# Kernel tuning notes

Measured on AMD Instinct MI355X. Metric: run time of the kernel, lower is better.

Reference implementation:

```python
import jax, jax.numpy as jnp
import numpy as np

ANGLE_SCALE = 100.0
DIST_SCALE = 100.0
DIST_BOUNDARY = 0.0
HID = 128
N_HIDDEN = 2  # output_layer
EPS = 1e-08


def _mlp(x, w0, b0, ws, bs):
    # Linear, then N_HIDDEN x (ReLU, Linear)
    h = x @ w0 + b0
    for i in range(ws.shape[0]):
        h = jax.nn.relu(h) @ ws[i] + bs[i]
    return h


def _capsule_endpoints(x):
    # x: [..., 9] -> A, B endpoints of capsule segment, radius r
    c, s = jnp.cos(x[..., 3:4] * ANGLE_SCALE), jnp.sin(x[..., 3:4] * ANGLE_SCALE)
    half = x[..., 2:3] / 2
    ctr = x[..., 0:2]
    off = jnp.concatenate([half * c, half * s], axis=-1)
    return ctr - off, ctr + off, x[..., 4:5]


def _pt_seg_dist(P, A, AB, AB_sq):
    t = jnp.clip(((P - A) * AB).sum(-1, keepdims=True) / AB_sq, 0.0, 1.0)
    Q = A + t * AB
    return jnp.linalg.norm(P - Q, axis=-1, keepdims=True)


def _dist_to_capsule(init_e, query_e):
    A1, B1, r1 = _capsule_endpoints(init_e)
    A2, B2, r2 = _capsule_endpoints(query_e)
    A1B1, A2B2 = B1 - A1, B2 - A2
    s1 = (A1B1 ** 2).sum(-1, keepdims=True) + EPS
    s2 = (A2B2 ** 2).sum(-1, keepdims=True) + EPS
    d = jnp.minimum(
        jnp.minimum(_pt_seg_dist(A2, A1, A1B1, s1), _pt_seg_dist(B2, A1, A1B1, s1)),
        jnp.minimum(_pt_seg_dist(A1, A2, A2B2, s2), _pt_seg_dist(B1, A2, A2B2, s2)),
    )
    return d - r1 - r2


def setup_inputs() -> dict:
    key = jax.random.key(0)
    ks = jax.random.split(key, 32)
    B, O, T = 64, 64, 64
    f = lambda k, shp, scale=1.0: jax.random.normal(k, shp, dtype=jnp.float32) * scale
    inp = {
        'init_x': f(ks[0], (B, O, 9)),
        'query_x': f(ks[1], (B, T, 9)),
        'init_v': f(ks[2], (B, O, 2)),
        'query_v': f(ks[3], (B, T, 2)),
        'init_angular_v': f(ks[4], (B, O, 1)),
        'query_angular_v': f(ks[5], (B, T, 1)),
        'trunk_w0': f(ks[6], (9, HID), 0.3), 'trunk_b0': f(ks[7], (HID,), 0.1),
        'trunk_ws': f(ks[8], (N_HIDDEN, HID, HID), 0.08), 'trunk_bs': f(ks[9], (N_HIDDEN, HID), 0.1),
        'branch_w0': f(ks[10], (5, HID), 0.3), 'branch_b0': f(ks[11], (HID,), 0.1),
        'branch_ws': f(ks[12], (N_HIDDEN, HID, HID), 0.08), 'branch_bs': f(ks[13], (N_HIDDEN, HID), 0.1),
        'out_w': f(ks[14], (HID, 3), 0.08), 'out_b': f(ks[15], (3,), 0.1),
        'spring_w0': f(ks[16], (1, HID), 0.3), 'spring_b0': f(ks[17], (HID,), 0.1),
        'spring_w1': f(ks[18], (HID, 1), 0.08), 'spring_b1': f(ks[19], (1,), 0.1),
        'joint_w0': f(ks[20], (15, HID), 0.3), 'joint_b0': f(ks[21], (HID,), 0.1),
        'joint_w1': f(ks[22], (HID, 2), 0.08), 'joint_b1': f(ks[23], (2,), 0.1),
    }
    return inp


def reference(init_x, query_x, init_v, query_v, init_angular_v, query_angular_v,
              trunk_w0, trunk_b0, trunk_ws, trunk_bs,
              branch_w0, branch_b0, branch_ws, branch_bs,
              out_w, out_b, spring_w0, spring_b0, spring_w1, spring_b1,
              joint_w0, joint_b0, joint_w1, joint_b1):
    B, O, _ = init_x.shape
    T = query_x.shape[1]
    # pairwise broadcast: init along obj axis (dim1), query along target axis (dim2)
    init_e = jnp.broadcast_to(init_x[:, :, None, :], (B, O, T, 9))
    query_e = jnp.broadcast_to(query_x[:, None, :, :], (B, O, T, 9))
    rel = query_e[..., :2] - init_e[..., :2]
    query_e = jnp.concatenate([rel, query_e[..., 2:]], axis=-1)
    init_e = jnp.concatenate([jnp.zeros_like(rel), init_e[..., 2:]], axis=-1)
    qv = query_v[:, None, :, :] - init_v[:, :, None, :]           # [B,O,T,2]
    qav = query_angular_v[:, None, :, :] - init_angular_v[:, :, None, :]  # [B,O,T,1]
    iav = jnp.broadcast_to(init_angular_v[:, :, None, :], (B, O, T, 1))

    dist = _dist_to_capsule(init_e, query_e)
    dist_mask = (dist <= DIST_BOUNDARY).astype(jnp.float32)
    dist_input = dist * dist_mask * DIST_SCALE

    branch_in = init_e[..., :5]
    trunk_in = jnp.concatenate([query_e[..., :5], qv, qav, dist_input], axis=-1)
    branch_out = _mlp(branch_in, branch_w0, branch_b0, branch_ws, branch_bs)
    trunk_out = _mlp(trunk_in, trunk_w0, trunk_b0, trunk_ws, trunk_bs)
    force = (branch_out * trunk_out) @ out_w + out_b  # [B,O,T,3]

    # spring force
    have_spring = ((init_e[..., 8:9] == query_e[..., 8:9]) & (init_e[..., 8:9] > 0)).astype(jnp.float32)
    dvec = init_e[..., :2] - query_e[..., :2]
    length = jnp.linalg.norm(dvec, axis=-1, keepdims=True)
    dvec = dvec / (length + EPS)
    sf = jax.nn.relu(length @ spring_w0 + spring_b0) @ spring_w1 + spring_b1  # [B,O,T,1]
    sf = sf * dvec
    sf = jnp.concatenate([sf, jnp.zeros_like(sf[..., :1])], axis=-1) * have_spring

    # joint force (torch .long() truncates toward zero)
    i7, q7 = init_e[..., 7:8], query_e[..., 7:8]
    have_joint = ((jnp.trunc(i7) == jnp.trunc(q7)) & (i7 > 0)).astype(jnp.float32)
    joint_in = jnp.concatenate([init_e[..., :5], query_e[..., :5], qv, iav, qav, i7 - jnp.trunc(i7)], axis=-1)
    jf = jax.nn.relu(joint_in @ joint_w0 + joint_b0) @ joint_w1 + joint_b1  # [B,O,T,2]
    jf = jf * have_joint
    jf = jnp.concatenate([jf, jnp.zeros_like(jf[..., :1])], axis=-1)

    force = force * dist_mask + sf + jf
    return force
```

## Files before the change

kernel.cpp:

```cpp
#include <hip/hip_runtime.h>
#include <math.h>


typedef _Float16 h4v __attribute__((ext_vector_type(4)));
typedef _Float16 h8v __attribute__((ext_vector_type(8)));
typedef float    f4v __attribute__((ext_vector_type(4)));
typedef unsigned int u32;

#define TW0_OFF 0
#define JW0_OFF 4096
#define TWS_OFF 8192
#define BW0_OFF 40960
#define BWS_OFF 45056
#define W_TOTAL 77824
#define BR_OFF_F (W_TOTAL/2)

#define FRAG_BLOCKS 304
#define BR_BLOCKS   256

__global__ __launch_bounds__(256)
void prep_kernel(const float* __restrict__ tw0, const float* __restrict__ tws,
                 const float* __restrict__ jw0, const float* __restrict__ bw0,
                 const float* __restrict__ bws, const float* __restrict__ bb0,
                 const float* __restrict__ bbs, const float* __restrict__ init_x,
                 _Float16* __restrict__ wsH, float* __restrict__ brw)
{
    __shared__ float bsm[2*16*132];
    const int tid = threadIdx.x;

    if (blockIdx.x < FRAG_BLOCKS) {
        int idx = blockIdx.x * 256 + tid;
        if (idx >= W_TOTAL) return;
        const int j = idx & 7;
        const int lane = (idx >> 3) & 63;
        const int q = lane >> 4, r = lane & 15;
        _Float16 v;
        if (idx < JW0_OFF) {
            int mt = idx >> 9;
            int k = q*8 + j, m = mt*16 + r;
            v = (k < 9) ? (_Float16)tw0[k*128 + m] : (_Float16)0.f;
        } else if (idx < TWS_OFF) {
            int mt = (idx - JW0_OFF) >> 9;
            int k = q*8 + j, m = mt*16 + r;
            v = (k < 15) ? (_Float16)jw0[k*128 + m] : (_Float16)0.f;
        } else if (idx < BW0_OFF) {
            int e = idx - TWS_OFF;
            int ks = (e >> 9) & 3, mt = (e >> 11) & 7, l = e >> 14;
            int k = ks*32 + q*8 + j, m = mt*16 + r;
            v = (_Float16)tws[l*16384 + k*128 + m];
        } else if (idx < BWS_OFF) {
            int mt = (idx - BW0_OFF) >> 9;
            int k = q*8 + j, m = mt*16 + r;
            v = (k < 5) ? (_Float16)bw0[k*128 + m] : (_Float16)0.f;
        } else {
            int e = idx - BWS_OFF;
            int ks = (e >> 9) & 3, mt = (e >> 11) & 7, l = e >> 14;
            int k = ks*32 + q*8 + j, m = mt*16 + r;
            v = (_Float16)bws[l*16384 + k*128 + m];
        }
        wsH[idx] = v;
        return;
    }

    const int blk2 = blockIdx.x - FRAG_BLOCKS;
    const int row0 = blk2*16;
    const int lane = tid & 63, w = tid >> 6;
    const int q = lane >> 4, r = lane & 15;
    float* h0 = bsm;
    float* h1 = bsm + 16*132;

    for (int e = tid; e < 2048; e += 256) {
        const int rw = e >> 7, n = e & 127;
        const float* ixp = init_x + (row0 + rw)*9;
        float acc = bb0[n];
        acc = fmaf(ixp[2], bw0[2*128 + n], acc);
        acc = fmaf(ixp[3], bw0[3*128 + n], acc);
        acc = fmaf(ixp[4], bw0[4*128 + n], acc);
        h0[rw*132 + n] = acc;
    }
    __syncthreads();

    #pragma unroll
    for (int L = 0; L < 2; ++L) {
        const float* Wg = bws + L*16384;
        const float* bi = bbs + L*128;
        const float* in = (L == 0) ? h0 : h1;
        #pragma unroll
        for (int mi = 0; mi < 2; ++mi) {
            const int mt = w + mi*4;
            const int m0 = mt*16 + q*4;
            h8v af[4];
            #pragma unroll
            for (int ks = 0; ks < 4; ++ks)
                #pragma unroll
                for (int j = 0; j < 8; ++j)
                    af[ks][j] = (_Float16)Wg[(ks*32 + q*8 + j)*128 + mt*16 + r];
            f4v acc = *(const f4v*)&bi[m0];
            #pragma unroll
            for (int ks = 0; ks < 4; ++ks) {
                f4v x0 = *(const f4v*)&in[r*132 + ks*32 + q*8];
                f4v x1 = *(const f4v*)&in[r*132 + ks*32 + q*8 + 4];
                h8v bf;
                #pragma unroll
                for (int i = 0; i < 4; ++i) {
                    bf[i]   = (_Float16)fmaxf(x0[i], 0.f);
                    bf[4+i] = (_Float16)fmaxf(x1[i], 0.f);
                }
                acc = __builtin_amdgcn_mfma_f32_16x16x32_f16(af[ks], bf, acc, 0, 0, 0);
            }
            if (L == 0)
                *(f4v*)&h1[r*132 + m0] = acc;
            else
                *(f4v*)&brw[(row0 + r)*128 + m0] = acc;
        }
        __syncthreads();
    }
}

__device__ __forceinline__ u32 sh_u32(u32 v, int idx) {
    return (u32)__shfl((int)v, idx, 64);
}
__device__ __forceinline__ h8v make_h8(u32 a, u32 b, u32 c, u32 d) {
    union { u32 u[4]; h8v h; } t;
    t.u[0] = a; t.u[1] = b; t.u[2] = c; t.u[3] = d;
    return t.h;
}
__device__ __forceinline__ u32 pack_relu2(float x, float y) {
    union { _Float16 h[2]; u32 u; } t;
    t.h[0] = (_Float16)fmaxf(x, 0.f);
    t.h[1] = (_Float16)fmaxf(y, 0.f);
    return t.u;
}

#define BUILD_BF(dst, P) do {                                                 \
    _Pragma("unroll")                                                         \
    for (int ks_ = 0; ks_ < 4; ++ks_) {                                       \
        u32 lo0 = sh_u32((P)[2*ks_][0],   idxA);                              \
        u32 hi0 = sh_u32((P)[2*ks_+1][0], idxA);                              \
        u32 lo1 = sh_u32((P)[2*ks_][1],   idxA);                              \
        u32 hi1 = sh_u32((P)[2*ks_+1][1], idxA);                              \
        u32 lo2 = sh_u32((P)[2*ks_][0],   idxB);                              \
        u32 hi2 = sh_u32((P)[2*ks_+1][0], idxB);                              \
        u32 lo3 = sh_u32((P)[2*ks_][1],   idxB);                              \
        u32 hi3 = sh_u32((P)[2*ks_+1][1], idxB);                              \
        (dst)[ks_] = make_h8(hiSel ? hi0 : lo0, hiSel ? hi1 : lo1,            \
                             hiSel ? hi2 : lo2, hiSel ? hi3 : lo3);           \
    }                                                                         \
} while (0)

__global__ __launch_bounds__(64)
void ff_kernel(const float* __restrict__ init_x,  const float* __restrict__ query_x,
               const float* __restrict__ init_v,  const float* __restrict__ query_v,
               const float* __restrict__ init_av, const float* __restrict__ query_av,
               const float* __restrict__ tb0, const float* __restrict__ tbs,
               const float* __restrict__ out_w, const float* __restrict__ out_b,
               const float* __restrict__ sw0, const float* __restrict__ sb0,
               const float* __restrict__ sw1, const float* __restrict__ sb1,
               const float* __restrict__ jb0,
               const float* __restrict__ jw1, const float* __restrict__ jb1,
               const _Float16* __restrict__ wsH, const float* __restrict__ brw,
               float* __restrict__ out)
{
    const int lane = threadIdx.x;
    const int bid  = blockIdx.x;
    const int obid = bid >> 1;
    const int half = bid & 1;
    const int b    = obid >> 6;
    const int g    = lane >> 4, c = lane & 15;
    const int idxA = (g & 1)*32 + c;
    const int idxB = idxA + 16;
    const bool hiSel = (lane & 32) != 0;

    const float* ix = init_x + obid*9;
    const float ix0 = ix[0], ix1 = ix[1], ix2 = ix[2], ix3 = ix[3], ix4 = ix[4];
    const float ix7 = ix[7], ix8 = ix[8];
    float s1v, c1v; sincosf(ix3 * 100.f, &s1v, &c1v);
    const float hh1 = ix2 * 0.5f;
    const float o1x = hh1*c1v, o1y = hh1*s1v;
    const float A1x = -o1x, A1y = -o1y;
    const float ab1x = 2.f*o1x, ab1y = 2.f*o1y;
    const float s1sq = ab1x*ab1x + ab1y*ab1y + 1e-8f;
    const float iv0 = init_v[obid*2+0], iv1 = init_v[obid*2+1];
    const float iav = init_av[obid];
    const float i7t = truncf(ix7);
    const float fr7 = ix7 - i7t;

    u32  p[2][8][2];
    float mask_[2], dvx_[2], dvy_[2], hs_[2], hj_[2], len_[2];
    float jf0_[2], jf1_[2];

    #pragma unroll
    for (int ntl = 0; ntl < 2; ++ntl) {
        const int tq = (half*2 + ntl)*16 + c;
        const float* qx = query_x + (b*64 + tq)*9;
        const float qx0 = qx[0], qx1 = qx[1], qx2 = qx[2], qx3 = qx[3], qx4 = qx[4];
        const float qx7 = qx[7], qx8 = qx[8];
        const float rel0 = qx0 - ix0, rel1 = qx1 - ix1;

        float s2v, c2v; sincosf(qx3 * 100.f, &s2v, &c2v);
        const float hh2 = qx2 * 0.5f;
        const float o2x = hh2*c2v, o2y = hh2*s2v;
        const float A2x = rel0 - o2x, A2y = rel1 - o2y;
        const float B2x = rel0 + o2x, B2y = rel1 + o2y;
        const float ab2x = 2.f*o2x, ab2y = 2.f*o2y;
        const float s2sq = ab2x*ab2x + ab2y*ab2y + 1e-8f;

        float Px, Py, Ax, Ay, ABx, ABy, ss;
        if (g < 2) {
            Ax = A1x; Ay = A1y; ABx = ab1x; ABy = ab1y; ss = s1sq;
            Px = (g == 0) ? A2x : B2x;  Py = (g == 0) ? A2y : B2y;
        } else {
            Ax = A2x; Ay = A2y; ABx = ab2x; ABy = ab2y; ss = s2sq;
            Px = (g == 2) ? A1x : o1x;  Py = (g == 2) ? A1y : o1y;
        }
        float t = ((Px - Ax)*ABx + (Py - Ay)*ABy) / ss;
        t = fminf(fmaxf(t, 0.f), 1.f);
        const float dx = Px - (Ax + t*ABx);
        const float dy = Py - (Ay + t*ABy);
        float dq = sqrtf(dx*dx + dy*dy);
        dq = fminf(dq, __shfl_xor(dq, 16));
        dq = fminf(dq, __shfl_xor(dq, 32));

        const float dist = dq - ix4 - qx4;
        const float mask = (dist <= 0.f) ? 1.f : 0.f;
        const float dinp = dist * mask * 100.f;
        const float qv0 = query_v[(b*64+tq)*2+0] - iv0;
        const float qv1 = query_v[(b*64+tq)*2+1] - iv1;
        const float qav = query_av[b*64+tq] - iav;
        const float len = sqrtf(rel0*rel0 + rel1*rel1);
        const float inv = 1.f / (len + 1e-8f);

        mask_[ntl] = mask;
        dvx_[ntl]  = -rel0 * inv;
        dvy_[ntl]  = -rel1 * inv;
        hs_[ntl]   = ((ix8 == qx8) && (ix8 > 0.f)) ? 1.f : 0.f;
        hj_[ntl]   = ((i7t == truncf(qx7)) && (ix7 > 0.f)) ? 1.f : 0.f;
        len_[ntl]  = len;

        const bool g0 = (g == 0), g1 = (g == 1);
        h8v bT, bJ;
        bT[0] = (_Float16)(g0 ? rel0 : g1 ? dinp : 0.f);
        bT[1] = (_Float16)(g0 ? rel1 : 0.f);
        bT[2] = (_Float16)(g0 ? qx2  : 0.f);
        bT[3] = (_Float16)(g0 ? qx3  : 0.f);
        bT[4] = (_Float16)(g0 ? qx4  : 0.f);
        bT[5] = (_Float16)(g0 ? qv0  : 0.f);
        bT[6] = (_Float16)(g0 ? qv1  : 0.f);
        bT[7] = (_Float16)(g0 ? qav  : 0.f);
        bJ[0] = (_Float16)(g1 ? qx3  : 0.f);
        bJ[1] = (_Float16)(g1 ? qx4  : 0.f);
        bJ[2] = (_Float16)(g0 ? ix2  : g1 ? qv0 : 0.f);
        bJ[3] = (_Float16)(g0 ? ix3  : g1 ? qv1 : 0.f);
        bJ[4] = (_Float16)(g0 ? ix4  : g1 ? iav : 0.f);
        bJ[5] = (_Float16)(g0 ? rel0 : g1 ? qav : 0.f);
        bJ[6] = (_Float16)(g0 ? rel1 : g1 ? fr7 : 0.f);
        bJ[7] = (_Float16)(g0 ? qx2  : 0.f);

        float jf0 = 0.f, jf1 = 0.f;
        #pragma unroll
        for (int mt = 0; mt < 8; ++mt) {
            const int m0 = mt*16 + g*4;
            h8v aT = *(const h8v*)&wsH[TW0_OFF + (mt*64 + lane)*8];
            f4v accT = *(const f4v*)&tb0[m0];
            accT = __builtin_amdgcn_mfma_f32_16x16x32_f16(aT, bT, accT, 0, 0, 0);
            p[ntl][mt][0] = pack_relu2(accT[0], accT[1]);
            p[ntl][mt][1] = pack_relu2(accT[2], accT[3]);

            h8v aJ = *(const h8v*)&wsH[JW0_OFF + (mt*64 + lane)*8];
            f4v accJ = *(const f4v*)&jb0[m0];
            accJ = __builtin_amdgcn_mfma_f32_16x16x32_f16(aJ, bJ, accJ, 0, 0, 0);
            f4v jwa = *(const f4v*)&jw1[m0*2];
            f4v jwb = *(const f4v*)&jw1[m0*2 + 4];
            const float h0r = fmaxf(accJ[0], 0.f), h1r = fmaxf(accJ[1], 0.f);
            const float h2r = fmaxf(accJ[2], 0.f), h3r = fmaxf(accJ[3], 0.f);
            jf0 = fmaf(h0r, jwa[0], fmaf(h1r, jwa[2], fmaf(h2r, jwb[0], fmaf(h3r, jwb[2], jf0))));
            jf1 = fmaf(h0r, jwa[1], fmaf(h1r, jwa[3], fmaf(h2r, jwb[1], fmaf(h3r, jwb[3], jf1))));
        }
        jf0_[ntl] = jf0; jf1_[ntl] = jf1;
    }

    float sp_[2] = {0.f, 0.f};
    #pragma unroll
    for (int ch = 0; ch < 8; ++ch) {
        const int n0 = g*32 + ch*4;
        f4v w0v = *(const f4v*)&sw0[n0];
        f4v b0v = *(const f4v*)&sb0[n0];
        f4v w1v = *(const f4v*)&sw1[n0];
        #pragma unroll
        for (int i = 0; i < 4; ++i)
            #pragma unroll
            for (int ntl = 0; ntl < 2; ++ntl)
                sp_[ntl] = fmaf(fmaxf(fmaf(len_[ntl], w0v[i], b0v[i]), 0.f), w1v[i], sp_[ntl]);
    }

    {
        h8v bf[2][4];
        #pragma unroll
        for (int n2 = 0; n2 < 2; ++n2)
            BUILD_BF(bf[n2], p[n2]);
        #pragma unroll
        for (int mt = 0; mt < 8; ++mt) {
            h8v a0 = *(const h8v*)&wsH[TWS_OFF + ((mt*4 + 0)*64 + lane)*8];
            h8v a1 = *(const h8v*)&wsH[TWS_OFF + ((mt*4 + 1)*64 + lane)*8];
            h8v a2 = *(const h8v*)&wsH[TWS_OFF + ((mt*4 + 2)*64 + lane)*8];
            h8v a3 = *(const h8v*)&wsH[TWS_OFF + ((mt*4 + 3)*64 + lane)*8];
            f4v bias = *(const f4v*)&tbs[mt*16 + g*4];
            #pragma unroll
            for (int n2 = 0; n2 < 2; ++n2) {
                f4v acc = bias;
                acc = __builtin_amdgcn_mfma_f32_16x16x32_f16(a0, bf[n2][0], acc, 0, 0, 0);
                acc = __builtin_amdgcn_mfma_f32_16x16x32_f16(a1, bf[n2][1], acc, 0, 0, 0);
                acc = __builtin_amdgcn_mfma_f32_16x16x32_f16(a2, bf[n2][2], acc, 0, 0, 0);
                acc = __builtin_amdgcn_mfma_f32_16x16x32_f16(a3, bf[n2][3], acc, 0, 0, 0);
                p[n2][mt][0] = pack_relu2(acc[0], acc[1]);
                p[n2][mt][1] = pack_relu2(acc[2], acc[3]);
            }
        }
    }

    float f0_[2] = {0,0}, f1_[2] = {0,0}, f2_[2] = {0,0};
    {
        h8v bf[2][4];
        #pragma unroll
        for (int n2 = 0; n2 < 2; ++n2)
            BUILD_BF(bf[n2], p[n2]);
        #pragma unroll
        for (int mt = 0; mt < 8; ++mt) {
            const int m0 = mt*16 + g*4;
            h8v a0 = *(const h8v*)&wsH[TWS_OFF + 16384 + ((mt*4 + 0)*64 + lane)*8];
            h8v a1 = *(const h8v*)&wsH[TWS_OFF + 16384 + ((mt*4 + 1)*64 + lane)*8];
            h8v a2 = *(const h8v*)&wsH[TWS_OFF + 16384 + ((mt*4 + 2)*64 + lane)*8];
            h8v a3 = *(const h8v*)&wsH[TWS_OFF + 16384 + ((mt*4 + 3)*64 + lane)*8];
            f4v bias = *(const f4v*)&tbs[128 + m0];
            f4v brv  = *(const f4v*)&brw[obid*128 + m0];
            f4v oa = *(const f4v*)&out_w[m0*3];
            f4v ob = *(const f4v*)&out_w[m0*3 + 4];
            f4v oc = *(const f4v*)&out_w[m0*3 + 8];
            #pragma unroll
            for (int n2 = 0; n2 < 2; ++n2) {
                f4v acc = bias;
                acc = __builtin_amdgcn_mfma_f32_16x16x32_f16(a0, bf[n2][0], acc, 0, 0, 0);
                acc = __builtin_amdgcn_mfma_f32_16x16x32_f16(a1, bf[n2][1], acc, 0, 0, 0);
                acc = __builtin_amdgcn_mfma_f32_16x16x32_f16(a2, bf[n2][2], acc, 0, 0, 0);
                acc = __builtin_amdgcn_mfma_f32_16x16x32_f16(a3, bf[n2][3], acc, 0, 0, 0);
                const float pr0 = acc[0]*brv[0], pr1 = acc[1]*brv[1];
                const float pr2 = acc[2]*brv[2], pr3 = acc[3]*brv[3];
                f0_[n2] += pr0*oa[0] + pr1*oa[3] + pr2*ob[2] + pr3*oc[1];
                f1_[n2] += pr0*oa[1] + pr1*ob[0] + pr2*ob[3] + pr3*oc[2];
                f2_[n2] += pr0*oa[2] + pr1*ob[1] + pr2*oc[0] + pr3*oc[3];
            }
        }
    }

    const float obs0 = out_b[0], obs1 = out_b[1], obs2 = out_b[2];
    const float sb1v = sb1[0], jb1a = jb1[0], jb1b = jb1[1];
    #pragma unroll
    for (int ntl = 0; ntl < 2; ++ntl) {
        float v0 = f0_[ntl], v1 = f1_[ntl], v2 = f2_[ntl];
        float v3 = jf0_[ntl], v4 = jf1_[ntl], v5 = sp_[ntl];
        v0 += __shfl_xor(v0, 16); v0 += __shfl_xor(v0, 32);
        v1 += __shfl_xor(v1, 16); v1 += __shfl_xor(v1, 32);
        v2 += __shfl_xor(v2, 16); v2 += __shfl_xor(v2, 32);
        v3 += __shfl_xor(v3, 16); v3 += __shfl_xor(v3, 32);
        v4 += __shfl_xor(v4, 16); v4 += __shfl_xor(v4, 32);
        v5 += __shfl_xor(v5, 16); v5 += __shfl_xor(v5, 32);
        if (g == 0) {
            const float sf = (v5 + sb1v) * hs_[ntl];
            const float j0 = (v3 + jb1a) * hj_[ntl];
            const float j1 = (v4 + jb1b) * hj_[ntl];
            float* op = out + (obid*64 + (half*2 + ntl)*16 + c)*3;
            op[0] = (v0 + obs0)*mask_[ntl] + sf*dvx_[ntl] + j0;
            op[1] = (v1 + obs1)*mask_[ntl] + sf*dvy_[ntl] + j1;
            op[2] = (v2 + obs2)*mask_[ntl];
        }
    }
}

extern "C" void kernel_launch(void* const* d_in, const int* in_sizes, int n_in,
                              void* d_out, int out_size, void* d_ws, size_t ws_size,
                              hipStream_t stream) {
    (void)in_sizes; (void)n_in; (void)out_size; (void)ws_size;
    _Float16* wsH = (_Float16*)d_ws;
    float* brw = (float*)d_ws + BR_OFF_F;

    prep_kernel<<<dim3(FRAG_BLOCKS + BR_BLOCKS), dim3(256), 0, stream>>>(
        (const float*)d_in[6],
        (const float*)d_in[8],
        (const float*)d_in[20],
        (const float*)d_in[10],
        (const float*)d_in[12],
        (const float*)d_in[11],
        (const float*)d_in[13],
        (const float*)d_in[0],
        wsH, brw);
    ff_kernel<<<dim3(64*64*2), dim3(64), 0, stream>>>(
        (const float*)d_in[0],  (const float*)d_in[1],  (const float*)d_in[2],
        (const float*)d_in[3],  (const float*)d_in[4],  (const float*)d_in[5],
        (const float*)d_in[7],  (const float*)d_in[9],
        (const float*)d_in[14], (const float*)d_in[15],
        (const float*)d_in[16], (const float*)d_in[17],
        (const float*)d_in[18], (const float*)d_in[19],
        (const float*)d_in[21],
        (const float*)d_in[22], (const float*)d_in[23],
        wsH, brw, (float*)d_out);
}
```

Before: 185.4 us.

## Share weight fragments across both tiles and spill epilogue scalars to LDS

Restructures the first-layer loop so each trunk and joint weight fragment and bias is loaded once and fed to MFMAs for both query tiles, instead of reloading per tile. Per-element epilogue scalars (mask, direction, spring and joint flags) move from registers into a small shared-memory buffer written by one lane group. The launch bound gains a minimum-waves hint of 3 to push the compiler toward lower register use and higher occupancy. The cost is extra LDS traffic and a compiler-imposed register cap that could cause spills. No explicit barrier is needed since the block is one wavefront.

```diff
diff --git a/kernel.cpp b/kernel.cpp
--- a/kernel.cpp
+++ b/kernel.cpp
@@ -148,7 +148,7 @@
     }                                                                         \
 } while (0)
 
-__global__ __launch_bounds__(64)
+__global__ __launch_bounds__(64, 3)
 void ff_kernel(const float* __restrict__ init_x,  const float* __restrict__ query_x,
                const float* __restrict__ init_v,  const float* __restrict__ query_v,
                const float* __restrict__ init_av, const float* __restrict__ query_av,
@@ -161,6 +161,7 @@
                const _Float16* __restrict__ wsH, const float* __restrict__ brw,
                float* __restrict__ out)
 {
+    __shared__ float es[5*32];
     const int lane = threadIdx.x;
     const int bid  = blockIdx.x;
     const int obid = bid >> 1;
@@ -186,8 +187,8 @@
     const float fr7 = ix7 - i7t;
 
     u32  p[2][8][2];
-    float mask_[2], dvx_[2], dvy_[2], hs_[2], hj_[2], len_[2];
-    float jf0_[2], jf1_[2];
+    float len_[2];
+    h8v bT[2], bJ[2];
 
     #pragma unroll
     for (int ntl = 0; ntl < 2; ++ntl) {
@@ -229,54 +230,66 @@
         const float qav = query_av[b*64+tq] - iav;
         const float len = sqrtf(rel0*rel0 + rel1*rel1);
         const float inv = 1.f / (len + 1e-8f);
-
-        mask_[ntl] = mask;
-        dvx_[ntl]  = -rel0 * inv;
-        dvy_[ntl]  = -rel1 * inv;
-        hs_[ntl]   = ((ix8 == qx8) && (ix8 > 0.f)) ? 1.f : 0.f;
-        hj_[ntl]   = ((i7t == truncf(qx7)) && (ix7 > 0.f)) ? 1.f : 0.f;
-        len_[ntl]  = len;
+        len_[ntl] = len;
+
+        if (g == 0) {
+            es[0*32 + ntl*16 + c] = mask;
+            es[1*32 + ntl*16 + c] = -rel0 * inv;
+            es[2*32 + ntl*16 + c] = -rel1 * inv;
+            es[3*32 + ntl*16 + c] = ((ix8 == qx8) && (ix8 > 0.f)) ? 1.f : 0.f;
+            es[4*32 + ntl*16 + c] = ((i7t == truncf(qx7)) && (ix7 > 0.f)) ? 1.f : 0.f;
+        }
 
         const bool g0 = (g == 0), g1 = (g == 1);
-        h8v bT, bJ;
-        bT[0] = (_Float16)(g0 ? rel0 : g1 ? dinp : 0.f);
-        bT[1] = (_Float16)(g0 ? rel1 : 0.f);
-        bT[2] = (_Float16)(g0 ? qx2  : 0.f);
-        bT[3] = (_Float16)(g0 ? qx3  : 0.f);
-        bT[4] = (_Float16)(g0 ? qx4  : 0.f);
-        bT[5] = (_Float16)(g0 ? qv0  : 0.f);
-        bT[6] = (_Float16)(g0 ? qv1  : 0.f);
-        bT[7] = (_Float16)(g0 ? qav  : 0.f);
-        bJ[0] = (_Float16)(g1 ? qx3  : 0.f);
-        bJ[1] = (_Float16)(g1 ? qx4  : 0.f);
-        bJ[2] = (_Float16)(g0 ? ix2  : g1 ? qv0 : 0.f);
-        bJ[3] = (_Float16)(g0 ? ix3  : g1 ? qv1 : 0.f);
-        bJ[4] = (_Float16)(g0 ? ix4  : g1 ? iav : 0.f);
-        bJ[5] = (_Float16)(g0 ? rel0 : g1 ? qav : 0.f);
-        bJ[6] = (_Float16)(g0 ? rel1 : g1 ? fr7 : 0.f);
-        bJ[7] = (_Float16)(g0 ? qx2  : 0.f);
-
-        float jf0 = 0.f, jf1 = 0.f;
-        #pragma unroll
-        for (int mt = 0; mt < 8; ++mt) {
-            const int m0 = mt*16 + g*4;
-            h8v aT = *(const h8v*)&wsH[TW0_OFF + (mt*64 + lane)*8];
-            f4v accT = *(const f4v*)&tb0[m0];
-            accT = __builtin_amdgcn_mfma_f32_16x16x32_f16(aT, bT, accT, 0, 0, 0);
-            p[ntl][mt][0] = pack_relu2(accT[0], accT[1]);
-            p[ntl][mt][1] = pack_relu2(accT[2], accT[3]);
-
-            h8v aJ = *(const h8v*)&wsH[JW0_OFF + (mt*64 + lane)*8];
-            f4v accJ = *(const f4v*)&jb0[m0];
-            accJ = __builtin_amdgcn_mfma_f32_16x16x32_f16(aJ, bJ, accJ, 0, 0, 0);
-            f4v jwa = *(const f4v*)&jw1[m0*2];
-            f4v jwb = *(const f4v*)&jw1[m0*2 + 4];
-            const float h0r = fmaxf(accJ[0], 0.f), h1r = fmaxf(accJ[1], 0.f);
-            const float h2r = fmaxf(accJ[2], 0.f), h3r = fmaxf(accJ[3], 0.f);
-            jf0 = fmaf(h0r, jwa[0], fmaf(h1r, jwa[2], fmaf(h2r, jwb[0], fmaf(h3r, jwb[2], jf0))));
-            jf1 = fmaf(h0r, jwa[1], fmaf(h1r, jwa[3], fmaf(h2r, jwb[1], fmaf(h3r, jwb[3], jf1))));
-        }
-        jf0_[ntl] = jf0; jf1_[ntl] = jf1;
+        bT[ntl][0] = (_Float16)(g0 ? rel0 : g1 ? dinp : 0.f);
+        bT[ntl][1] = (_Float16)(g0 ? rel1 : 0.f);
+        bT[ntl][2] = (_Float16)(g0 ? qx2  : 0.f);
+        bT[ntl][3] = (_Float16)(g0 ? qx3  : 0.f);
+        bT[ntl][4] = (_Float16)(g0 ? qx4  : 0.f);
+        bT[ntl][5] = (_Float16)(g0 ? qv0  : 0.f);
+        bT[ntl][6] = (_Float16)(g0 ? qv1  : 0.f);
+        bT[ntl][7] = (_Float16)(g0 ? qav  : 0.f);
+        bJ[ntl][0] = (_Float16)(g1 ? qx3  : 0.f);
+        bJ[ntl][1] = (_Float16)(g1 ? qx4  : 0.f);
+        bJ[ntl][2] = (_Float16)(g0 ? ix2  : g1 ? qv0 : 0.f);
+        bJ[ntl][3] = (_Float16)(g0 ? ix3  : g1 ? qv1 : 0.f);
+        bJ[ntl][4] = (_Float16)(g0 ? ix4  : g1 ? iav : 0.f);
+        bJ[ntl][5] = (_Float16)(g0 ? rel0 : g1 ? qav : 0.f);
+        bJ[ntl][6] = (_Float16)(g0 ? rel1 : g1 ? fr7 : 0.f);
+        bJ[ntl][7] = (_Float16)(g0 ? qx2  : 0.f);
+    }
+
+    float jf0_[2] = {0.f, 0.f}, jf1_[2] = {0.f, 0.f};
+    #pragma unroll
+    for (int mt = 0; mt < 8; ++mt) {
+        const int m0 = mt*16 + g*4;
+        h8v aT = *(const h8v*)&wsH[TW0_OFF + (mt*64 + lane)*8];
+        f4v tb = *(const f4v*)&tb0[m0];
+        f4v acc0 = __builtin_amdgcn_mfma_f32_16x16x32_f16(aT, bT[0], tb, 0, 0, 0);
+        f4v acc1 = __builtin_amdgcn_mfma_f32_16x16x32_f16(aT, bT[1], tb, 0, 0, 0);
+        p[0][mt][0] = pack_relu2(acc0[0], acc0[1]);
+        p[0][mt][1] = pack_relu2(acc0[2], acc0[3]);
+        p[1][mt][0] = pack_relu2(acc1[0], acc1[1]);
+        p[1][mt][1] = pack_relu2(acc1[2], acc1[3]);
+
+        h8v aJ = *(const h8v*)&wsH[JW0_OFF + (mt*64 + lane)*8];
+        f4v jb = *(const f4v*)&jb0[m0];
+        f4v aj0 = __builtin_amdgcn_mfma_f32_16x16x32_f16(aJ, bJ[0], jb, 0, 0, 0);
+        f4v aj1 = __builtin_amdgcn_mfma_f32_16x16x32_f16(aJ, bJ[1], jb, 0, 0, 0);
+        f4v jwa = *(const f4v*)&jw1[m0*2];
+        f4v jwb = *(const f4v*)&jw1[m0*2 + 4];
+        {
+            const float h0r = fmaxf(aj0[0], 0.f), h1r = fmaxf(aj0[1], 0.f);
+            const float h2r = fmaxf(aj0[2], 0.f), h3r = fmaxf(aj0[3], 0.f);
+            jf0_[0] = fmaf(h0r, jwa[0], fmaf(h1r, jwa[2], fmaf(h2r, jwb[0], fmaf(h3r, jwb[2], jf0_[0]))));
+            jf1_[0] = fmaf(h0r, jwa[1], fmaf(h1r, jwa[3], fmaf(h2r, jwb[1], fmaf(h3r, jwb[3], jf1_[0]))));
+        }
+        {
+            const float h0r = fmaxf(aj1[0], 0.f), h1r = fmaxf(aj1[1], 0.f);
+            const float h2r = fmaxf(aj1[2], 0.f), h3r = fmaxf(aj1[3], 0.f);
+            jf0_[1] = fmaf(h0r, jwa[0], fmaf(h1r, jwa[2], fmaf(h2r, jwb[0], fmaf(h3r, jwb[2], jf0_[1]))));
+            jf1_[1] = fmaf(h0r, jwa[1], fmaf(h1r, jwa[3], fmaf(h2r, jwb[1], fmaf(h3r, jwb[3], jf1_[1]))));
+        }
     }
 
     float sp_[2] = {0.f, 0.f};
@@ -365,13 +378,18 @@
         v4 += __shfl_xor(v4, 16); v4 += __shfl_xor(v4, 32);
         v5 += __shfl_xor(v5, 16); v5 += __shfl_xor(v5, 32);
         if (g == 0) {
-            const float sf = (v5 + sb1v) * hs_[ntl];
-            const float j0 = (v3 + jb1a) * hj_[ntl];
-            const float j1 = (v4 + jb1b) * hj_[ntl];
+            const float mask = es[0*32 + ntl*16 + c];
+            const float dvx  = es[1*32 + ntl*16 + c];
+            const float dvy  = es[2*32 + ntl*16 + c];
+            const float hs   = es[3*32 + ntl*16 + c];
+            const float hj   = es[4*32 + ntl*16 + c];
+            const float sf = (v5 + sb1v) * hs;
+            const float j0 = (v3 + jb1a) * hj;
+            const float j1 = (v4 + jb1b) * hj;
             float* op = out + (obid*64 + (half*2 + ntl)*16 + c)*3;
-            op[0] = (v0 + obs0)*mask_[ntl] + sf*dvx_[ntl] + j0;
-            op[1] = (v1 + obs1)*mask_[ntl] + sf*dvy_[ntl] + j1;
-            op[2] = (v2 + obs2)*mask_[ntl];
+            op[0] = (v0 + obs0)*mask + sf*dvx + j0;
+            op[1] = (v1 + obs1)*mask + sf*dvy + j1;
+            op[2] = (v2 + obs2)*mask;
         }
     }
 }
```

Result: slower. 313.3 us (+69.0%).
